# Performance work log

Hardware: AMD Instinct MI355X
Metric: run time of the kernel (lower is better)

The kernel has to match this reference:

```python
import jax, jax.numpy as jnp
import numpy as np

B, S, H, DH = 2, 4096, 8, 64
D = H * DH


def setup_inputs() -> dict:
    key = jax.random.key(0)
    ks = jax.random.split(key, 6)
    std = 1.0 / np.sqrt(D)
    return {
        "x": jax.random.normal(ks[0], (B, S, D), dtype=jnp.float32),
        "Wq": jax.random.normal(ks[1], (D, D), dtype=jnp.float32) * std,
        "Wk": jax.random.normal(ks[2], (D, D), dtype=jnp.float32) * std,
        "Wv": jax.random.normal(ks[3], (D, D), dtype=jnp.float32) * std,
        "Wo": jax.random.normal(ks[4], (D, D), dtype=jnp.float32) * std,
        "bo": jnp.zeros((D,), dtype=jnp.float32),
    }


def reference(x, Wq, Wk, Wv, Wo, bo):
    scale = DH ** (-0.5)
    # torch Linear: y = x @ W.T
    q = x @ Wq.T  # [B,S,D]
    k = x @ Wk.T
    v = x @ Wv.T
    # split heads -> [B,H,S,Dh]
    q = q.reshape(B, S, H, DH).transpose(0, 2, 1, 3)
    k = k.reshape(B, S, H, DH).transpose(0, 2, 1, 3)
    v = v.reshape(B, S, H, DH).transpose(0, 2, 1, 3)
    score = jnp.einsum('bhqd,bhkd->bhqk', q, k) * scale  # [B,H,S,S]
    weights = jax.nn.softmax(score, axis=-1)
    attn = jnp.einsum('bhqk,bhkd->bhqd', weights, v)  # [B,H,S,Dh]
    h_ = attn.transpose(0, 2, 1, 3).reshape(B, S, D)
    return h_ @ Wo.T + bo
```

## Files before the change

kernel.cpp:

```cpp
#include <hip/hip_runtime.h>

#define LOG2E 1.44269504088896340736f

typedef unsigned short u16;
typedef __bf16 bf16x4_t __attribute__((ext_vector_type(4)));
typedef __bf16 bf16x8_t __attribute__((ext_vector_type(8)));
typedef float f32x4_t __attribute__((ext_vector_type(4)));

__device__ __forceinline__ u16 f2bf(float f) {
  union { float f; unsigned int u; } v;
  v.f = f;
  unsigned int u = v.u;
  u += 0x7fffu + ((u >> 16) & 1u);
  return (u16)(u >> 16);
}

__device__ __forceinline__ f32x4_t mfma16(bf16x8_t a, bf16x8_t b, f32x4_t c) {
  return __builtin_amdgcn_mfma_f32_16x16x32_bf16(a, b, c, 0, 0, 0);
}

__device__ __forceinline__ void gl_lds16(const u16* g, u16* l) {
  __builtin_amdgcn_global_load_lds(
      (const __attribute__((address_space(1))) unsigned int*)g,
      (__attribute__((address_space(3))) unsigned int*)l, 16, 0, 0);
}

__global__ __launch_bounds__(256) void cast_all_kernel(
    const float* __restrict__ x, const float* __restrict__ wq, const float* __restrict__ wk,
    const float* __restrict__ wv, const float* __restrict__ wo,
    u16* __restrict__ xb, u16* __restrict__ wqb, u16* __restrict__ wkb,
    u16* __restrict__ wvb, u16* __restrict__ wob) {
  const int NX = 2 * 4096 * 512;
  const int NW = 512 * 512;
  int i = (blockIdx.x * 256 + threadIdx.x) * 4;
  const float* src; u16* dst; int off; float scale = 1.f;
  if (i < NX)               { src = x;  dst = xb;  off = i; }
  else if (i < NX + NW)     { src = wq; dst = wqb; off = i - NX; scale = 0.125f * LOG2E; }
  else if (i < NX + 2 * NW) { src = wk; dst = wkb; off = i - NX - NW; }
  else if (i < NX + 3 * NW) { src = wv; dst = wvb; off = i - NX - 2 * NW; }
  else                      { src = wo; dst = wob; off = i - NX - 3 * NW; }
  float4 f = *(const float4*)(src + off);
  unsigned int lo = (unsigned int)f2bf(f.x * scale) | ((unsigned int)f2bf(f.y * scale) << 16);
  unsigned int hi = (unsigned int)f2bf(f.z * scale) | ((unsigned int)f2bf(f.w * scale) << 16);
  uint2 o; o.x = lo; o.y = hi;
  *(uint2*)(dst + off) = o;
}

template <int MODE>
__device__ __forceinline__ void gemm_core(const u16* __restrict__ A, const u16* __restrict__ Bt,
                                          void* __restrict__ Cout, const float* __restrict__ bias,
                                          int Mbase, int Nbase) {
  __shared__ __align__(16) u16 As[128][40];
  __shared__ __align__(16) u16 Bs[128][40];
  const int t = threadIdx.x;
  const int wave = t >> 6, lane = t & 63;
  const int r = lane & 15, qd = lane >> 4;
  const int wm = wave & 1, wn = wave >> 1;
  const int lr = t >> 2;
  const int lc = (t & 3) * 8;

  f32x4_t acc[4][4];
#pragma unroll
  for (int i = 0; i < 4; i++)
#pragma unroll
    for (int j = 0; j < 4; j++) { f32x4_t z = {0.f, 0.f, 0.f, 0.f}; acc[i][j] = z; }

  const u16* pa0 = A  + (Mbase + lr) * 512 + lc;
  const u16* pa1 = A  + (Mbase + 64 + lr) * 512 + lc;
  const u16* pb0 = Bt + (Nbase + lr) * 512 + lc;
  const u16* pb1 = Bt + (Nbase + 64 + lr) * 512 + lc;

  uint4 ra0 = *(const uint4*)(pa0);
  uint4 ra1 = *(const uint4*)(pa1);
  uint4 rb0 = *(const uint4*)(pb0);
  uint4 rb1 = *(const uint4*)(pb1);

  for (int k0 = 0; k0 < 512; k0 += 32) {
    *(uint4*)&As[lr][lc]      = ra0;
    *(uint4*)&As[64 + lr][lc] = ra1;
    *(uint4*)&Bs[lr][lc]      = rb0;
    *(uint4*)&Bs[64 + lr][lc] = rb1;
    __syncthreads();
    if (k0 < 480) {
      ra0 = *(const uint4*)(pa0 + k0 + 32);
      ra1 = *(const uint4*)(pa1 + k0 + 32);
      rb0 = *(const uint4*)(pb0 + k0 + 32);
      rb1 = *(const uint4*)(pb1 + k0 + 32);
    }
    bf16x8_t af[4], bfr[4];
#pragma unroll
    for (int i = 0; i < 4; i++) af[i]  = *(const bf16x8_t*)&As[wm * 64 + i * 16 + r][qd * 8];
#pragma unroll
    for (int j = 0; j < 4; j++) bfr[j] = *(const bf16x8_t*)&Bs[wn * 64 + j * 16 + r][qd * 8];
#pragma unroll
    for (int i = 0; i < 4; i++)
#pragma unroll
      for (int j = 0; j < 4; j++) acc[i][j] = mfma16(af[i], bfr[j], acc[i][j]);
    __syncthreads();
  }

  float bv[4];
  if (MODE == 2) {
#pragma unroll
    for (int j = 0; j < 4; j++) bv[j] = bias[Nbase + wn * 64 + j * 16 + r];
  }
#pragma unroll
  for (int i = 0; i < 4; i++) {
#pragma unroll
    for (int reg = 0; reg < 4; reg++) {
      int gr = Mbase + wm * 64 + i * 16 + qd * 4 + reg;
#pragma unroll
      for (int j = 0; j < 4; j++) {
        int gc = Nbase + wn * 64 + j * 16 + r;
        float val = acc[i][j][reg];
        if (MODE == 2) {
          ((float*)Cout)[gr * 512 + gc] = val + bv[j];
        } else if (MODE == 1) {
          int bb = gc >> 12, ss = gc & 4095;
          ((__bf16*)Cout)[((long)(bb * 512 + gr)) * 4096 + ss] = (__bf16)val;
        } else {
          ((__bf16*)Cout)[gr * 512 + gc] = (__bf16)val;
        }
      }
    }
  }
}

__global__ __launch_bounds__(256) void gemm_qkv_kernel(
    const u16* __restrict__ X,
    const u16* __restrict__ Wq, const u16* __restrict__ Wk, const u16* __restrict__ Wv,
    u16* __restrict__ Q, u16* __restrict__ K, u16* __restrict__ Vt) {
  if (blockIdx.z == 0)
    gemm_core<0>(X, Wq, Q, nullptr, blockIdx.x * 128, blockIdx.y * 128);
  else if (blockIdx.z == 1)
    gemm_core<0>(X, Wk, K, nullptr, blockIdx.x * 128, blockIdx.y * 128);
  else
    gemm_core<1>(Wv, X, Vt, nullptr, blockIdx.y * 128, blockIdx.x * 128);
}

__global__ __launch_bounds__(256) void gemm_out_kernel(
    const u16* __restrict__ Aat, const u16* __restrict__ Wo,
    float* __restrict__ Out, const float* __restrict__ bo) {
  gemm_core<2>(Aat, Wo, Out, bo, blockIdx.x * 128, blockIdx.y * 128);
}

__global__ __launch_bounds__(256, 2) void attn_kernel(
    const u16* __restrict__ Q, const u16* __restrict__ K, const u16* __restrict__ Vt,
    u16* __restrict__ Oattn) {
  __shared__ __align__(16) u16 Ks[2][2][4096];
  __shared__ __align__(16) u16 Vs[2][2][4096];
  __shared__ __align__(16) u16 Ps[4][2048];

  const int t = threadIdx.x;
  const int wave = t >> 6, lane = t & 63;
  const int r = lane & 15, qd = lane >> 4;
  const int g = wave & 1, kv = wave >> 1;
  const int bh = blockIdx.y;
  const int b = bh >> 3, h = bh & 7;
  const long bbase = (long)b * 4096 * 512;
  const int q0 = blockIdx.x * 128;

  const int sw = r & 7;
  const int ck0 = (qd ^ sw) * 8;
  const int ck1 = ((qd + 4) ^ sw) * 8;
  const int psw = r & 3;
  const int pck = (qd ^ psw) * 8;

  bf16x8_t qf[4][2];
#pragma unroll
  for (int qa = 0; qa < 4; qa++) {
    const u16* qp = Q + bbase + (long)(q0 + g * 64 + qa * 16 + r) * 512 + h * 64 + qd * 8;
    qf[qa][0] = *(const bf16x8_t*)(qp);
    qf[qa][1] = *(const bf16x8_t*)(qp + 32);
  }

  f32x4_t accO[4][4];
  float Lacc[4];
#pragma unroll
  for (int qa = 0; qa < 4; qa++) {
    f32x4_t z = {0.f, 0.f, 0.f, 0.f};
    Lacc[qa] = 0.f;
#pragma unroll
    for (int nt = 0; nt < 4; nt++) accO[qa][nt] = z;
  }

  const int rr = lane >> 3;
  const int cc = (lane & 7) ^ rr;
  const u16* kgb = K + bbase + (long)(kv * 2048 + g * 32 + rr) * 512 + h * 64 + cc * 8;
  const u16* vgb = Vt + ((long)(b * 512 + h * 64 + g * 32 + rr)) * 4096 + kv * 2048 + cc * 8;

#pragma unroll
  for (int i = 0; i < 4; i++) gl_lds16(kgb + (long)i * 8 * 512, &Ks[kv][0][g * 2048] + i * 512);
#pragma unroll
  for (int i = 0; i < 4; i++) gl_lds16(vgb + i * 8 * 4096, &Vs[kv][0][g * 2048] + i * 512);

  for (int it = 0; it < 32; it++) {
    const int buf = it & 1;
    __syncthreads();

    if (it < 31) {
      const int nb = (it + 1) & 1;
      const long ko = (long)(it + 1) * 64;
#pragma unroll
      for (int i = 0; i < 4; i++)
        gl_lds16(kgb + (ko + i * 8) * 512, &Ks[kv][nb][g * 2048] + i * 512);
#pragma unroll
      for (int i = 0; i < 4; i++)
        gl_lds16(vgb + ko + (long)i * 8 * 4096, &Vs[kv][nb][g * 2048] + i * 512);
    }

    bf16x8_t kf[4][2];
#pragma unroll
    for (int nt = 0; nt < 4; nt++) {
      const u16* kb = &Ks[kv][buf][(nt * 16 + r) * 64];
      kf[nt][0] = *(const bf16x8_t*)(kb + ck0);
      kf[nt][1] = *(const bf16x8_t*)(kb + ck1);
    }

    f32x4_t St[4][4];
#pragma unroll
    for (int qa = 0; qa < 4; qa++)
#pragma unroll
      for (int nt = 0; nt < 4; nt++) {
        f32x4_t z = {0.f, 0.f, 0.f, 0.f};
        z = mfma16(kf[nt][0], qf[qa][0], z);
        z = mfma16(kf[nt][1], qf[qa][1], z);
        St[qa][nt] = z;
      }

    bf16x4_t pk[4][4];
#pragma unroll
    for (int qa = 0; qa < 4; qa++)
#pragma unroll
      for (int nt = 0; nt < 4; nt++) {
        float p0 = __builtin_amdgcn_exp2f(St[qa][nt][0]);
        float p1 = __builtin_amdgcn_exp2f(St[qa][nt][1]);
        float p2 = __builtin_amdgcn_exp2f(St[qa][nt][2]);
        float p3 = __builtin_amdgcn_exp2f(St[qa][nt][3]);
        Lacc[qa] += (p0 + p1) + (p2 + p3);
        pk[qa][nt][0] = (__bf16)p0; pk[qa][nt][1] = (__bf16)p1;
        pk[qa][nt][2] = (__bf16)p2; pk[qa][nt][3] = (__bf16)p3;
      }

#pragma unroll
    for (int ks = 0; ks < 2; ks++) {
#pragma unroll
      for (int qa = 0; qa < 4; qa++)
#pragma unroll
        for (int nh = 0; nh < 2; nh++) {
          int slot = ((nh * 2 + (qd >> 1)) ^ psw);
          *(uint2*)&Ps[wave][(qa * 16 + r) * 32 + slot * 8 + (qd & 1) * 4] =
              *(uint2*)&pk[qa][ks * 2 + nh];
        }
      bf16x8_t pf[4];
#pragma unroll
      for (int qa = 0; qa < 4; qa++)
        pf[qa] = *(const bf16x8_t*)&Ps[wave][(qa * 16 + r) * 32 + pck];
#pragma unroll
      for (int nt = 0; nt < 4; nt++) {
        const u16* vb = &Vs[kv][buf][(nt * 16 + r) * 64];
        bf16x8_t vf = *(const bf16x8_t*)(vb + (ks ? ck1 : ck0));
#pragma unroll
        for (int qa = 0; qa < 4; qa++)
          accO[qa][nt] = mfma16(pf[qa], vf, accO[qa][nt]);
      }
    }
  }

  __syncthreads();
  float* Sc  = (float*)&Ks[0][0][0];
  float* Lsc = (float*)&Vs[0][0][0];
  if (kv == 1) {
#pragma unroll
    for (int qa = 0; qa < 4; qa++) {
#pragma unroll
      for (int nt = 0; nt < 4; nt++)
        *(f32x4_t*)&Sc[g * 4096 + ((qa * 4 + nt) * 64 + lane) * 4] = accO[qa][nt];
      Lsc[g * 256 + qa * 64 + lane] = Lacc[qa];
    }
  }
  __syncthreads();
  if (kv == 0) {
#pragma unroll
    for (int qa = 0; qa < 4; qa++) {
      Lacc[qa] += Lsc[g * 256 + qa * 64 + lane];
      float v = Lacc[qa];
      v += __shfl_xor(v, 16);
      v += __shfl_xor(v, 32);
      Lacc[qa] = v;
#pragma unroll
      for (int nt = 0; nt < 4; nt++) {
        f32x4_t o = *(const f32x4_t*)&Sc[g * 4096 + ((qa * 4 + nt) * 64 + lane) * 4];
        accO[qa][nt] += o;
      }
    }
#pragma unroll
    for (int qa = 0; qa < 4; qa++)
#pragma unroll
      for (int reg = 0; reg < 4; reg++) {
        float L = __shfl(Lacc[qa], qd * 4 + reg);
        float inv = 1.f / L;
        int gr = q0 + g * 64 + qa * 16 + qd * 4 + reg;
#pragma unroll
        for (int nt = 0; nt < 4; nt++)
          ((__bf16*)Oattn)[bbase + (long)gr * 512 + h * 64 + nt * 16 + r] =
              (__bf16)(accO[qa][nt][reg] * inv);
      }
  }
}

extern "C" void kernel_launch(void* const* d_in, const int* in_sizes, int n_in,
                              void* d_out, int out_size, void* d_ws, size_t ws_size,
                              hipStream_t stream) {
  const float* x  = (const float*)d_in[0];
  const float* Wq = (const float*)d_in[1];
  const float* Wk = (const float*)d_in[2];
  const float* Wv = (const float*)d_in[3];
  const float* Wo = (const float*)d_in[4];
  const float* bo = (const float*)d_in[5];
  float* out = (float*)d_out;

  u16* ws  = (u16*)d_ws;
  u16* xb  = ws;
  u16* wqb = xb  + 4194304;
  u16* wkb = wqb + 262144;
  u16* wvb = wkb + 262144;
  u16* wob = wvb + 262144;
  u16* Qb  = wob + 262144;
  u16* Kb  = Qb  + 4194304;
  u16* Vtg = Kb  + 4194304;
  u16* Ab  = Vtg + 4194304;

  cast_all_kernel<<<5120, 256, 0, stream>>>(x, Wq, Wk, Wv, Wo, xb, wqb, wkb, wvb, wob);

  dim3 g1(64, 4, 3);
  gemm_qkv_kernel<<<g1, 256, 0, stream>>>(xb, wqb, wkb, wvb, Qb, Kb, Vtg);

  dim3 g2(32, 16);
  attn_kernel<<<g2, 256, 0, stream>>>(Qb, Kb, Vtg, Ab);

  dim3 g3(64, 4);
  gemm_out_kernel<<<g3, 256, 0, stream>>>(Ab, wob, out, bo);
}
```

Baseline: 211.5 us.

## Feed P directly from registers into PV MFMA using 16x16x16 transposed layout

Removes the per-wave LDS staging buffer for softmax probabilities. The S^T accumulator layout from the QK MFMA is reused directly as the B operand of a 16x16x16 bf16 MFMA, with V as the A operand, so the output accumulator becomes transposed (dim x query). The epilogue is rewritten to match: each lane writes four contiguous bf16 values per row, and the per-row shuffle of the normalizer goes away. The cost is twice as many smaller-K MFMA instructions and narrower 8-byte V reads from LDS, in exchange for dropping LDS writes, reads and the associated latency.

```diff
diff --git a/kernel.cpp b/kernel.cpp
--- a/kernel.cpp
+++ b/kernel.cpp
@@ -3,6 +3,7 @@
 #define LOG2E 1.44269504088896340736f
 
 typedef unsigned short u16;
+typedef short s16x4 __attribute__((ext_vector_type(4)));
 typedef __bf16 bf16x4_t __attribute__((ext_vector_type(4)));
 typedef __bf16 bf16x8_t __attribute__((ext_vector_type(8)));
 typedef float f32x4_t __attribute__((ext_vector_type(4)));
@@ -17,6 +18,9 @@
 
 __device__ __forceinline__ f32x4_t mfma16(bf16x8_t a, bf16x8_t b, f32x4_t c) {
   return __builtin_amdgcn_mfma_f32_16x16x32_bf16(a, b, c, 0, 0, 0);
+}
+__device__ __forceinline__ f32x4_t mfma16x16(s16x4 a, s16x4 b, f32x4_t c) {
+  return __builtin_amdgcn_mfma_f32_16x16x16bf16_1k(a, b, c, 0, 0, 0);
 }
 
 __device__ __forceinline__ void gl_lds16(const u16* g, u16* l) {
@@ -149,7 +153,6 @@
     u16* __restrict__ Oattn) {
   __shared__ __align__(16) u16 Ks[2][2][4096];
   __shared__ __align__(16) u16 Vs[2][2][4096];
-  __shared__ __align__(16) u16 Ps[4][2048];
 
   const int t = threadIdx.x;
   const int wave = t >> 6, lane = t & 63;
@@ -163,8 +166,10 @@
   const int sw = r & 7;
   const int ck0 = (qd ^ sw) * 8;
   const int ck1 = ((qd + 4) ^ sw) * 8;
-  const int psw = r & 3;
-  const int pck = (qd ^ psw) * 8;
+  int vck[4];
+#pragma unroll
+  for (int ks = 0; ks < 4; ks++)
+    vck[ks] = ((ks * 2 + (qd >> 1)) ^ sw) * 8 + (qd & 1) * 4;
 
   bf16x8_t qf[4][2];
 #pragma unroll
@@ -228,7 +233,7 @@
         St[qa][nt] = z;
       }
 
-    bf16x4_t pk[4][4];
+    s16x4 pk[4][4];
 #pragma unroll
     for (int qa = 0; qa < 4; qa++)
 #pragma unroll
@@ -238,32 +243,22 @@
         float p2 = __builtin_amdgcn_exp2f(St[qa][nt][2]);
         float p3 = __builtin_amdgcn_exp2f(St[qa][nt][3]);
         Lacc[qa] += (p0 + p1) + (p2 + p3);
-        pk[qa][nt][0] = (__bf16)p0; pk[qa][nt][1] = (__bf16)p1;
-        pk[qa][nt][2] = (__bf16)p2; pk[qa][nt][3] = (__bf16)p3;
+        bf16x4_t pb;
+        pb[0] = (__bf16)p0; pb[1] = (__bf16)p1; pb[2] = (__bf16)p2; pb[3] = (__bf16)p3;
+        pk[qa][nt] = *(s16x4*)&pb;
       }
 
 #pragma unroll
-    for (int ks = 0; ks < 2; ks++) {
+    for (int ks = 0; ks < 4; ks++) {
+      s16x4 va[4];
+#pragma unroll
+      for (int dm = 0; dm < 4; dm++)
+        va[dm] = *(const s16x4*)&Vs[kv][buf][(dm * 16 + r) * 64 + vck[ks]];
 #pragma unroll
       for (int qa = 0; qa < 4; qa++)
 #pragma unroll
-        for (int nh = 0; nh < 2; nh++) {
-          int slot = ((nh * 2 + (qd >> 1)) ^ psw);
-          *(uint2*)&Ps[wave][(qa * 16 + r) * 32 + slot * 8 + (qd & 1) * 4] =
-              *(uint2*)&pk[qa][ks * 2 + nh];
-        }
-      bf16x8_t pf[4];
-#pragma unroll
-      for (int qa = 0; qa < 4; qa++)
-        pf[qa] = *(const bf16x8_t*)&Ps[wave][(qa * 16 + r) * 32 + pck];
-#pragma unroll
-      for (int nt = 0; nt < 4; nt++) {
-        const u16* vb = &Vs[kv][buf][(nt * 16 + r) * 64];
-        bf16x8_t vf = *(const bf16x8_t*)(vb + (ks ? ck1 : ck0));
-#pragma unroll
-        for (int qa = 0; qa < 4; qa++)
-          accO[qa][nt] = mfma16(pf[qa], vf, accO[qa][nt]);
-      }
+        for (int dm = 0; dm < 4; dm++)
+          accO[qa][dm] = mfma16x16(va[dm], pk[qa][ks], accO[qa][dm]);
     }
   }
 
@@ -274,8 +269,8 @@
 #pragma unroll
     for (int qa = 0; qa < 4; qa++) {
 #pragma unroll
-      for (int nt = 0; nt < 4; nt++)
-        *(f32x4_t*)&Sc[g * 4096 + ((qa * 4 + nt) * 64 + lane) * 4] = accO[qa][nt];
+      for (int dm = 0; dm < 4; dm++)
+        *(f32x4_t*)&Sc[g * 4096 + ((qa * 4 + dm) * 64 + lane) * 4] = accO[qa][dm];
       Lsc[g * 256 + qa * 64 + lane] = Lacc[qa];
     }
   }
@@ -288,24 +283,21 @@
       v += __shfl_xor(v, 16);
       v += __shfl_xor(v, 32);
       Lacc[qa] = v;
-#pragma unroll
-      for (int nt = 0; nt < 4; nt++) {
-        f32x4_t o = *(const f32x4_t*)&Sc[g * 4096 + ((qa * 4 + nt) * 64 + lane) * 4];
-        accO[qa][nt] += o;
+    }
+#pragma unroll
+    for (int qa = 0; qa < 4; qa++) {
+      float inv = 1.f / Lacc[qa];
+      int gq = q0 + g * 64 + qa * 16 + r;
+#pragma unroll
+      for (int dm = 0; dm < 4; dm++) {
+        f32x4_t o = *(const f32x4_t*)&Sc[g * 4096 + ((qa * 4 + dm) * 64 + lane) * 4];
+        o += accO[qa][dm];
+        bf16x4_t ob;
+#pragma unroll
+        for (int reg = 0; reg < 4; reg++) ob[reg] = (__bf16)(o[reg] * inv);
+        *(uint2*)&Oattn[bbase + (long)gq * 512 + h * 64 + dm * 16 + qd * 4] = *(uint2*)&ob;
       }
     }
-#pragma unroll
-    for (int qa = 0; qa < 4; qa++)
-#pragma unroll
-      for (int reg = 0; reg < 4; reg++) {
-        float L = __shfl(Lacc[qa], qd * 4 + reg);
-        float inv = 1.f / L;
-        int gr = q0 + g * 64 + qa * 16 + qd * 4 + reg;
-#pragma unroll
-        for (int nt = 0; nt < 4; nt++)
-          ((__bf16*)Oattn)[bbase + (long)gr * 512 + h * 64 + nt * 16 + r] =
-              (__bf16)(accO[qa][nt][reg] * inv);
-      }
   }
 }
 
```

Result: faster. 197.1 us (-6.8%).
